# Performance work log

Measured on AMD Instinct MI355X. Metric: run time of the kernel, lower is better.

## Reference

```python
import jax, jax.numpy as jnp
import numpy as np

T, M, D_TRAJ, D_TEXT = 2048, 32, 256, 768
TAU = 1.0
LN_EPS = 1e-5

def _ln(x, g, b):
    mu = jnp.mean(x, axis=-1, keepdims=True)
    var = jnp.mean(jnp.square(x - mu), axis=-1, keepdims=True)
    return (x - mu) * jax.lax.rsqrt(var + LN_EPS) * g + b

def _gelu(x):
    return jax.nn.gelu(x, approximate=False)  # torch nn.GELU default (erf)

def _gcn_layer(x, src, dst, w, dst_scale, ln_g, ln_b, W, bb, N):
    h = _ln(x, ln_g, ln_b)
    m = h @ W + bb                      # [N, D]
    msg = m[src] * w[:, None]           # gather + weight  [E, D]
    out = jax.ops.segment_sum(msg, dst, num_segments=N)  # scatter-add
    deg = jax.ops.segment_sum(w, dst, num_segments=N)
    out = out / jnp.maximum(deg, 1.0)[:, None]
    out = out * dst_scale[:, None]
    return x + _gelu(out)

def setup_inputs() -> dict:
    key = jax.random.key(0)
    ks = jax.random.split(key, 12)
    traj_tokens = jax.random.normal(ks[0], (T, D_TRAJ), jnp.float32)
    word_tokens = jax.random.normal(ks[1], (M, D_TEXT), jnp.float32)
    t = jnp.arange(T - 1, dtype=jnp.int64)
    edge_index_temporal = jnp.stack([t, t + 1])                 # chain i->i+1
    ts = jnp.repeat(jnp.arange(T, dtype=jnp.int64), M)          # traj src
    ws = jnp.tile(jnp.arange(M, dtype=jnp.int64), T) + T        # word dst (offset T)
    edge_index_semantic = jnp.stack([ts, ws])
    s = 0.02
    params = {
        'W1': jax.random.normal(ks[2], (D_TRAJ, D_TEXT), jnp.float32) * s,
        'b1': jnp.zeros((D_TEXT,), jnp.float32),
        'W2': jax.random.normal(ks[3], (D_TEXT, D_TEXT), jnp.float32) * s,
        'b2': jnp.zeros((D_TEXT,), jnp.float32),
        'ln_g': jnp.ones((D_TEXT,), jnp.float32),
        'ln_b': jnp.zeros((D_TEXT,), jnp.float32),
        'traj_scale': jnp.asarray(0.2, jnp.float32),
        'g0_ln_g': jnp.ones((D_TEXT,), jnp.float32),
        'g0_ln_b': jnp.zeros((D_TEXT,), jnp.float32),
        'g0_W': jax.random.normal(ks[4], (D_TEXT, D_TEXT), jnp.float32) * s,
        'g0_b': jnp.zeros((D_TEXT,), jnp.float32),
        'g1_ln_g': jnp.ones((D_TEXT,), jnp.float32),
        'g1_ln_b': jnp.zeros((D_TEXT,), jnp.float32),
        'g1_W': jax.random.normal(ks[5], (D_TEXT, D_TEXT), jnp.float32) * s,
        'g1_b': jnp.zeros((D_TEXT,), jnp.float32),
    }
    return dict(traj_tokens=traj_tokens, word_tokens=word_tokens,
                edge_index_temporal=edge_index_temporal,
                edge_index_semantic=edge_index_semantic,
                valid_len=1536, **params)

def reference(traj_tokens, word_tokens, edge_index_temporal, edge_index_semantic,
              valid_len, W1, b1, W2, b2, ln_g, ln_b, traj_scale,
              g0_ln_g, g0_ln_b, g0_W, g0_b, g1_ln_g, g1_ln_b, g1_W, g1_b):
    N = T + M
    # traj projection MLP -> LN -> clamped learned scale
    z = _gelu(traj_tokens @ W1 + b1) @ W2 + b2
    z0 = _ln(z, ln_g, ln_b) * jnp.clip(traj_scale, 0.05, 2.0)
    h_init = jnp.concatenate([z0, word_tokens], axis=0)  # [N, D]
    # temporal edge weights gated by valid_len
    E_temp = edge_index_temporal.shape[1]
    w_temp = (jnp.arange(E_temp) < (valid_len - 1)).astype(jnp.float32)
    # semantic alignment: softmax over words per valid traj token
    zn = z0[:valid_len]
    zn = zn / jnp.maximum(jnp.linalg.norm(zn, axis=-1, keepdims=True), 1e-12)
    wn = word_tokens / jnp.maximum(jnp.linalg.norm(word_tokens, axis=-1, keepdims=True), 1e-12)
    alpha = jax.nn.softmax(zn @ wn.T / max(TAU, 1e-6), axis=1)   # [valid, M]
    alpha_full = jnp.concatenate(
        [alpha, jnp.zeros((T - valid_len, M), alpha.dtype)], axis=0)
    w_sem = alpha_full.reshape(-1)                               # [T*M]
    beta = alpha.sum(axis=0)
    inv_beta = jnp.clip(1.0 / (jax.lax.stop_gradient(beta) + 1e-6), 0.2, 5.0)
    dst_scale = jnp.concatenate([jnp.ones((T,), jnp.float32), inv_beta])
    # combined edge list + weights
    src = jnp.concatenate([edge_index_temporal[0], edge_index_semantic[0]])
    dst = jnp.concatenate([edge_index_temporal[1], edge_index_semantic[1]])
    w_all = jnp.concatenate([w_temp, w_sem])
    # 2-layer local DiWeightedGCN
    h = _gcn_layer(h_init, src, dst, w_all, dst_scale, g0_ln_g, g0_ln_b, g0_W, g0_b, N)
    h = _gcn_layer(h, src, dst, w_all, dst_scale, g1_ln_g, g1_ln_b, g1_W, g1_b, N)
    return h  # h_loc [T+M, D_TEXT]
```

## Files before the change

kernel.cpp:

```cpp
#include <hip/hip_runtime.h>
#include <math.h>

#define T_NODES 2048
#define M_WORDS 32
#define D 768
#define DTRAJ 256
#define NCHUNK 128

typedef __attribute__((ext_vector_type(8))) short bhalf8;
typedef __attribute__((ext_vector_type(4))) float f32x4;

#define AS1 __attribute__((address_space(1)))
#define AS3 __attribute__((address_space(3)))

constexpr size_t OFF_A1HI = 0;
constexpr size_t OFF_A1LO = OFF_A1HI + (size_t)T_NODES * DTRAJ * 2;
constexpr size_t OFF_AHI  = OFF_A1LO + (size_t)T_NODES * DTRAJ * 2;
constexpr size_t OFF_ALO  = OFF_AHI + (size_t)T_NODES * D * 2;
constexpr size_t OFF_WT1H = OFF_ALO + (size_t)T_NODES * D * 2;
constexpr size_t OFF_WT1L = OFF_WT1H + (size_t)D * DTRAJ * 2;
constexpr size_t OFF_WT2H = OFF_WT1L + (size_t)D * DTRAJ * 2;
constexpr size_t OFF_WT2L = OFF_WT2H + (size_t)D * D * 2;
constexpr size_t OFF_WG0H = OFF_WT2L + (size_t)D * D * 2;
constexpr size_t OFF_WG0L = OFF_WG0H + (size_t)D * D * 2;
constexpr size_t OFF_WG1H = OFF_WG0L + (size_t)D * D * 2;
constexpr size_t OFF_WG1L = OFF_WG1H + (size_t)D * D * 2;
constexpr size_t OFF_BUFB = OFF_WG1L + (size_t)D * D * 2;
constexpr size_t OFF_ALPH = OFF_BUFB + (size_t)T_NODES * D * 4;
constexpr size_t OFF_WPRT = OFF_ALPH + (size_t)T_NODES * M_WORDS * 4;
constexpr size_t OFF_BPRT = OFF_WPRT + (size_t)NCHUNK * M_WORDS * D * 4;
constexpr size_t OFF_INVW = OFF_BPRT + (size_t)NCHUNK * M_WORDS * 4;

__device__ __forceinline__ float gelu_exact(float x) {
    return 0.5f * x * (1.0f + erff(x * 0.70710678118654752f));
}
__device__ __forceinline__ unsigned short f2bf(float x) {
    unsigned int u = __float_as_uint(x);
    return (unsigned short)((u + 0x7fffu + ((u >> 16) & 1u)) >> 16);
}
__device__ __forceinline__ float bf2f(unsigned short b) {
    return __uint_as_float(((unsigned int)b) << 16);
}
__device__ __forceinline__ void stage16(const unsigned short* g, short* l) {
    __builtin_amdgcn_global_load_lds((const AS1 void*)g, (AS3 void*)l, 16, 0, 0);
}

__device__ __forceinline__ float wave_reduce_sum(float v) {
#pragma unroll
    for (int off = 32; off > 0; off >>= 1) v += __shfl_down(v, off);
    return v;
}
__device__ __forceinline__ float block_reduce_sum256(float v, float* sbuf) {
    v = wave_reduce_sum(v);
    const int lane = threadIdx.x & 63, wid = threadIdx.x >> 6;
    if (lane == 0) sbuf[wid] = v;
    __syncthreads();
    float r = sbuf[0] + sbuf[1] + sbuf[2] + sbuf[3];
    __syncthreads();
    return r;
}

__device__ __forceinline__ void ln_row(const float* __restrict__ x,
                                       const float* __restrict__ g,
                                       const float* __restrict__ b, float* sbuf,
                                       float& y0, float& y1, float& y2) {
    const int tid = threadIdx.x;
    const float x0 = x[tid], x1 = x[tid + 256], x2 = x[tid + 512];
    const float s = block_reduce_sum256(x0 + x1 + x2, sbuf);
    const float mu = s * (1.0f / 768.0f);
    const float d0 = x0 - mu, d1 = x1 - mu, d2 = x2 - mu;
    const float v = block_reduce_sum256(d0 * d0 + d1 * d1 + d2 * d2, sbuf);
    const float rs = rsqrtf(v * (1.0f / 768.0f) + 1e-5f);
    y0 = d0 * rs * g[tid] + b[tid];
    y1 = d1 * rs * g[tid + 256] + b[tid + 256];
    y2 = d2 * rs * g[tid + 512] + b[tid + 512];
}

__device__ __forceinline__ void tr_split_tile2(const float* __restrict__ W,
                                               unsigned short* __restrict__ hi,
                                               unsigned short* __restrict__ lo, int K,
                                               int N, int n0, int k0, float* tile) {
    const int tx = threadIdx.x & 31, ty = threadIdx.x >> 5;
#pragma unroll
    for (int i = 0; i < 32; i += 8)
        tile[(ty + i) * 33 + tx] = W[(size_t)(k0 + ty + i) * N + n0 + tx];
    __syncthreads();
#pragma unroll
    for (int i = 0; i < 32; i += 8) {
        const float v = tile[tx * 33 + ty + i];
        const unsigned short h = f2bf(v);
        const size_t o = (size_t)(n0 + ty + i) * K + k0 + tx;
        hi[o] = h;
        lo[o] = f2bf(v - bf2f(h));
    }
}

__global__ __launch_bounds__(256) void prep_kernel(
    const float* __restrict__ traj, const float* __restrict__ W1,
    const float* __restrict__ W2, const float* __restrict__ Wg0,
    const float* __restrict__ Wg1, const float* __restrict__ words,
    unsigned short* __restrict__ A1hi, unsigned short* __restrict__ A1lo,
    unsigned short* __restrict__ WT1h, unsigned short* __restrict__ WT1l,
    unsigned short* __restrict__ WT2h, unsigned short* __restrict__ WT2l,
    unsigned short* __restrict__ WG0h, unsigned short* __restrict__ WG0l,
    unsigned short* __restrict__ WG1h, unsigned short* __restrict__ WG1l,
    float* __restrict__ invw) {
    __shared__ float tile[32 * 33];
    __shared__ float sbuf[4];
    const int blk = blockIdx.x;
    if (blk < 512) {
        const int i = (blk * 256 + threadIdx.x) * 4;
        const float4 v = *(const float4*)(traj + i);
        ushort4 h, l;
        h.x = f2bf(v.x); l.x = f2bf(v.x - bf2f(h.x));
        h.y = f2bf(v.y); l.y = f2bf(v.y - bf2f(h.y));
        h.z = f2bf(v.z); l.z = f2bf(v.z - bf2f(h.z));
        h.w = f2bf(v.w); l.w = f2bf(v.w - bf2f(h.w));
        *(ushort4*)(A1hi + i) = h;
        *(ushort4*)(A1lo + i) = l;
    } else if (blk < 704) {
        const int idx = blk - 512;
        tr_split_tile2(W1, WT1h, WT1l, DTRAJ, D, (idx % 24) * 32, (idx / 24) * 32, tile);
    } else if (blk < 2432) {
        const int idx = blk - 704;
        const int wsel = idx / 576, rem = idx % 576;
        const float* W = (wsel == 0) ? W2 : (wsel == 1) ? Wg0 : Wg1;
        unsigned short* hi = (wsel == 0) ? WT2h : (wsel == 1) ? WG0h : WG1h;
        unsigned short* lo = (wsel == 0) ? WT2l : (wsel == 1) ? WG0l : WG1l;
        tr_split_tile2(W, hi, lo, D, D, (rem % 24) * 32, (rem / 24) * 32, tile);
    } else {
        const int w = blk - 2432;
        const size_t src = (size_t)w * D + threadIdx.x;
        const float x0 = words[src], x1 = words[src + 256], x2 = words[src + 512];
        const float ss = block_reduce_sum256(x0 * x0 + x1 * x1 + x2 * x2, sbuf);
        if (threadIdx.x == 0) invw[w] = 1.0f / fmaxf(sqrtf(ss), 1e-12f);
    }
}

#define MFMA_BF16(a, b, c) __builtin_amdgcn_mfma_f32_16x16x32_bf16(a, b, c, 0, 0, 0)

template <int EPI, bool TRIM>
__global__ __launch_bounds__(128) void mfma_gemm(
    const unsigned short* __restrict__ Ahi, const unsigned short* __restrict__ Alo,
    const unsigned short* __restrict__ Bthi, const unsigned short* __restrict__ Btlo,
    const float* __restrict__ bias, float* __restrict__ C,
    unsigned short* __restrict__ Ohi, unsigned short* __restrict__ Olo, int K_,
    const int* __restrict__ vlp) {
    const int bm = blockIdx.x * 64;
    if (TRIM && bm >= *vlp) return;
    __shared__ short sA[2][2][64 * 32];
    __shared__ short sB[2][2][96 * 32];
    const int bn = blockIdx.y * 96;
    const int tid = threadIdx.x;
    const int wv = tid >> 6, lane = tid & 63;
    const int lrow = lane >> 2;
    const int lchunk = (((lane & 3) ^ ((lrow >> 1) & 3)) << 3);
    const int g = lane >> 4, r = lane & 15;
    const int aoff = ((g ^ ((r >> 1) & 3)) << 3);
    const int wn = wv * 48;

    f32x4 acc[4][3];
#pragma unroll
    for (int i = 0; i < 4; ++i)
#pragma unroll
        for (int j = 0; j < 3; ++j) acc[i][j] = (f32x4){0.f, 0.f, 0.f, 0.f};

#define STAGE(buf, k0)                                                                     \
    if (wv == 0) {                                                                         \
        _Pragma("unroll") for (int i = 0; i < 4; ++i)                                      \
            stage16(Ahi + (size_t)(bm + i * 16 + lrow) * K_ + (k0) + lchunk,               \
                    &sA[buf][0][i * 512]);                                                 \
        _Pragma("unroll") for (int i = 0; i < 4; ++i)                                      \
            stage16(Alo + (size_t)(bm + i * 16 + lrow) * K_ + (k0) + lchunk,               \
                    &sA[buf][1][i * 512]);                                                 \
        _Pragma("unroll") for (int i = 0; i < 2; ++i)                                      \
            stage16(Bthi + (size_t)(bn + i * 16 + lrow) * K_ + (k0) + lchunk,              \
                    &sB[buf][0][i * 512]);                                                 \
    } else {                                                                               \
        _Pragma("unroll") for (int i = 2; i < 6; ++i)                                      \
            stage16(Bthi + (size_t)(bn + i * 16 + lrow) * K_ + (k0) + lchunk,              \
                    &sB[buf][0][i * 512]);                                                 \
        _Pragma("unroll") for (int i = 0; i < 6; ++i)                                      \
            stage16(Btlo + (size_t)(bn + i * 16 + lrow) * K_ + (k0) + lchunk,              \
                    &sB[buf][1][i * 512]);                                                 \
    }

    const int NT = K_ >> 5;
    STAGE(0, 0)
    __syncthreads();
    int cur = 0;
    for (int kt = 0; kt < NT; ++kt) {
        if (kt + 1 < NT) { STAGE(cur ^ 1, (kt + 1) << 5) }
        bhalf8 af[4][2];
#pragma unroll
        for (int fm = 0; fm < 4; ++fm) {
            af[fm][0] = *(const bhalf8*)(void*)&sA[cur][0][(fm * 16 + r) * 32 + aoff];
            af[fm][1] = *(const bhalf8*)(void*)&sA[cur][1][(fm * 16 + r) * 32 + aoff];
        }
#pragma unroll
        for (int fn = 0; fn < 3; ++fn) {
            const bhalf8 bh = *(const bhalf8*)(void*)&sB[cur][0][(wn + fn * 16 + r) * 32 + aoff];
            const bhalf8 bl = *(const bhalf8*)(void*)&sB[cur][1][(wn + fn * 16 + r) * 32 + aoff];
#pragma unroll
            for (int fm = 0; fm < 4; ++fm) {
                acc[fm][fn] = MFMA_BF16(af[fm][0], bh, acc[fm][fn]);
                acc[fm][fn] = MFMA_BF16(af[fm][0], bl, acc[fm][fn]);
                acc[fm][fn] = MFMA_BF16(af[fm][1], bh, acc[fm][fn]);
            }
        }
        __syncthreads();
        cur ^= 1;
    }
#undef STAGE

#pragma unroll
    for (int fm = 0; fm < 4; ++fm)
#pragma unroll
        for (int fn = 0; fn < 3; ++fn) {
            const int col = bn + wn + fn * 16 + r;
            const float bv = bias[col];
#pragma unroll
            for (int j = 0; j < 4; ++j) {
                const int row = bm + fm * 16 + g * 4 + j;
                float v = acc[fm][fn][j] + bv;
                if (EPI == 0) {
                    C[(size_t)row * D + col] = v;
                } else {
                    v = gelu_exact(v);
                    const unsigned short h = f2bf(v);
                    Ohi[(size_t)row * D + col] = h;
                    Olo[(size_t)row * D + col] = f2bf(v - bf2f(h));
                }
            }
        }
}

__global__ __launch_bounds__(256) void init_softmax(
    const float* __restrict__ z, const float* __restrict__ g,
    const float* __restrict__ b, const float* __restrict__ tsp,
    const float* __restrict__ words, const float* __restrict__ invw,
    const int* __restrict__ vlp, float* __restrict__ h, float* __restrict__ alpha) {
    __shared__ float sbuf[4];
    __shared__ float row[D];
    __shared__ float logits[M_WORDS];
    const int blk = blockIdx.x, tid = threadIdx.x;
    if (blk >= T_NODES) {
        const int w = blk - T_NODES;
        const size_t src = (size_t)w * D + tid;
        const size_t dst = (size_t)(T_NODES + w) * D + tid;
        h[dst] = words[src];
        h[dst + 256] = words[src + 256];
        h[dst + 512] = words[src + 512];
        return;
    }
    float y0, y1, y2;
    ln_row(z + (size_t)blk * D, g, b, sbuf, y0, y1, y2);
    const float sc = fminf(fmaxf(tsp[0], 0.05f), 2.0f);
    y0 *= sc; y1 *= sc; y2 *= sc;
    const size_t o = (size_t)blk * D + tid;
    h[o] = y0; h[o + 256] = y1; h[o + 512] = y2;
    const float ss = block_reduce_sum256(y0 * y0 + y1 * y1 + y2 * y2, sbuf);
    const float iz = 1.0f / fmaxf(sqrtf(ss), 1e-12f);
    if (blk >= *vlp) return;
    row[tid] = y0; row[tid + 256] = y1; row[tid + 512] = y2;
    __syncthreads();
    const int wid = tid >> 6, lane = tid & 63;
#pragma unroll
    for (int i = 0; i < 8; ++i) {
        const int w = wid * 8 + i;
        const float* wr = words + (size_t)w * D;
        float dot = 0.0f;
        for (int e = lane; e < D; e += 64) dot = fmaf(row[e], wr[e], dot);
        dot = wave_reduce_sum(dot);
        if (lane == 0) logits[w] = dot * iz * invw[w];
    }
    __syncthreads();
    if (tid < 64) {
        const float val = (tid < 32) ? logits[tid] : -INFINITY;
        float mx = val;
#pragma unroll
        for (int off = 32; off > 0; off >>= 1) mx = fmaxf(mx, __shfl_xor(mx, off));
        const float e = (tid < 32) ? expf(val - mx) : 0.0f;
        float sum = e;
#pragma unroll
        for (int off = 32; off > 0; off >>= 1) sum += __shfl_xor(sum, off);
        if (tid < 32) alpha[(size_t)blk * M_WORDS + tid] = e / sum;
    }
}

template <int FIN>
__global__ __launch_bounds__(256) void ln_split_fin(
    const float* __restrict__ x, const float* __restrict__ g,
    const float* __restrict__ b, unsigned short* __restrict__ hi,
    unsigned short* __restrict__ lo, const float* __restrict__ wpart,
    const float* __restrict__ bpart, float* __restrict__ h) {
    __shared__ float sbuf[4];
    const int blk = blockIdx.x, tid = threadIdx.x;
    if (blk < T_NODES) {
        float y0, y1, y2;
        ln_row(x + (size_t)blk * D, g, b, sbuf, y0, y1, y2);
        const size_t o = (size_t)blk * D + tid;
        unsigned short hh;
        hh = f2bf(y0); hi[o] = hh;       lo[o] = f2bf(y0 - bf2f(hh));
        hh = f2bf(y1); hi[o + 256] = hh; lo[o + 256] = f2bf(y1 - bf2f(hh));
        hh = f2bf(y2); hi[o + 512] = hh; lo[o + 512] = f2bf(y2 - bf2f(hh));
    } else if (FIN) {
        const int w = blk - T_NODES;
        float bsum = (tid < NCHUNK) ? bpart[tid * M_WORDS + w] : 0.0f;
        const float beta = block_reduce_sum256(bsum, sbuf);
        const float ib = fminf(fmaxf(1.0f / (beta + 1e-6f), 0.2f), 5.0f);
        const float scl = ib / fmaxf(beta, 1.0f);
#pragma unroll
        for (int i = 0; i < 3; ++i) {
            const int c = tid + i * 256;
            float acc = 0.0f;
#pragma unroll 8
            for (int q = 0; q < NCHUNK; ++q)
                acc += wpart[((size_t)q * M_WORDS + w) * D + c];
            h[(size_t)(T_NODES + w) * D + c] += gelu_exact(acc * scl);
        }
    }
}

__global__ __launch_bounds__(256) void gcn_agg_kernel(const float* __restrict__ m,
                                                      const float* __restrict__ alpha,
                                                      const int* __restrict__ vlp,
                                                      float* __restrict__ h,
                                                      float* __restrict__ wpart,
                                                      float* __restrict__ bpart) {
    const int VL = *vlp;
    const int chunk = blockIdx.x, cb = blockIdx.y;
    const int c = cb * 256 + threadIdx.x;
    const int tpc = (VL + NCHUNK - 1) / NCHUNK;
    const int t0 = chunk * tpc;
    const int t1 = min(t0 + tpc, VL);
    float acc[M_WORDS] = {};
    for (int t = t0; t < t1; ++t) {
        const float mv = m[(size_t)t * D + c];
        if (t + 1 < VL) h[(size_t)(t + 1) * D + c] += gelu_exact(mv);
        const float4* a4 = (const float4*)(alpha + (size_t)t * M_WORDS);
#pragma unroll
        for (int q = 0; q < 8; ++q) {
            const float4 a = a4[q];
            acc[q * 4 + 0] = fmaf(a.x, mv, acc[q * 4 + 0]);
            acc[q * 4 + 1] = fmaf(a.y, mv, acc[q * 4 + 1]);
            acc[q * 4 + 2] = fmaf(a.z, mv, acc[q * 4 + 2]);
            acc[q * 4 + 3] = fmaf(a.w, mv, acc[q * 4 + 3]);
        }
    }
#pragma unroll
    for (int w = 0; w < M_WORDS; ++w)
        wpart[((size_t)chunk * M_WORDS + w) * D + c] = acc[w];
    if (cb == 0 && threadIdx.x < M_WORDS) {
        float bs = 0.0f;
        for (int t = t0; t < t1; ++t) bs += alpha[(size_t)t * M_WORDS + threadIdx.x];
        bpart[chunk * M_WORDS + threadIdx.x] = bs;
    }
}

__global__ __launch_bounds__(256) void word_fin_kernel(const float* __restrict__ wpart,
                                                       const float* __restrict__ bpart,
                                                       float* __restrict__ h) {
    const int idx = blockIdx.x * 256 + threadIdx.x;
    const int w = idx / D, c = idx - w * D;
    float beta = 0.0f, acc = 0.0f;
#pragma unroll 8
    for (int q = 0; q < NCHUNK; ++q) {
        beta += bpart[q * M_WORDS + w];
        acc += wpart[((size_t)q * M_WORDS + w) * D + c];
    }
    const float ib = fminf(fmaxf(1.0f / (beta + 1e-6f), 0.2f), 5.0f);
    const float v = acc / fmaxf(beta, 1.0f) * ib;
    h[(size_t)(T_NODES + w) * D + c] += gelu_exact(v);
}

extern "C" void kernel_launch(void* const* d_in, const int* in_sizes, int n_in,
                              void* d_out, int out_size, void* d_ws, size_t ws_size,
                              hipStream_t stream) {
    const float* traj = (const float*)d_in[0];
    const float* words = (const float*)d_in[1];
    const int* vlp = (const int*)d_in[4];
    const float* W1 = (const float*)d_in[5];
    const float* b1 = (const float*)d_in[6];
    const float* W2 = (const float*)d_in[7];
    const float* b2 = (const float*)d_in[8];
    const float* ln_g = (const float*)d_in[9];
    const float* ln_b = (const float*)d_in[10];
    const float* tsc = (const float*)d_in[11];
    const float* g_ln_g[2] = {(const float*)d_in[12], (const float*)d_in[16]};
    const float* g_ln_b[2] = {(const float*)d_in[13], (const float*)d_in[17]};
    const float* g_W[2] = {(const float*)d_in[14], (const float*)d_in[18]};
    const float* g_b[2] = {(const float*)d_in[15], (const float*)d_in[19]};

    char* wsb = (char*)d_ws;
    unsigned short* A1hi = (unsigned short*)(wsb + OFF_A1HI);
    unsigned short* A1lo = (unsigned short*)(wsb + OFF_A1LO);
    unsigned short* Ahi = (unsigned short*)(wsb + OFF_AHI);
    unsigned short* Alo = (unsigned short*)(wsb + OFF_ALO);
    unsigned short* WT1h = (unsigned short*)(wsb + OFF_WT1H);
    unsigned short* WT1l = (unsigned short*)(wsb + OFF_WT1L);
    unsigned short* WT2h = (unsigned short*)(wsb + OFF_WT2H);
    unsigned short* WT2l = (unsigned short*)(wsb + OFF_WT2L);
    unsigned short* WG0h = (unsigned short*)(wsb + OFF_WG0H);
    unsigned short* WG0l = (unsigned short*)(wsb + OFF_WG0L);
    unsigned short* WG1h = (unsigned short*)(wsb + OFF_WG1H);
    unsigned short* WG1l = (unsigned short*)(wsb + OFF_WG1L);
    float* bufB = (float*)(wsb + OFF_BUFB);
    float* alpha = (float*)(wsb + OFF_ALPH);
    float* wpart = (float*)(wsb + OFF_WPRT);
    float* bpart = (float*)(wsb + OFF_BPRT);
    float* invw = (float*)(wsb + OFF_INVW);
    float* h = (float*)d_out;

    const unsigned short* WGh[2] = {WG0h, WG1h};
    const unsigned short* WGl[2] = {WG0l, WG1l};

    const dim3 ggrid(T_NODES / 64, D / 96);

    prep_kernel<<<2464, 256, 0, stream>>>(traj, W1, W2, g_W[0], g_W[1], words, A1hi, A1lo,
                                          WT1h, WT1l, WT2h, WT2l, WG0h, WG0l, WG1h, WG1l,
                                          invw);
    mfma_gemm<1, false><<<ggrid, 128, 0, stream>>>(A1hi, A1lo, WT1h, WT1l, b1, nullptr,
                                                   Ahi, Alo, DTRAJ, vlp);
    mfma_gemm<0, false><<<ggrid, 128, 0, stream>>>(Ahi, Alo, WT2h, WT2l, b2, bufB,
                                                   nullptr, nullptr, D, vlp);
    init_softmax<<<T_NODES + M_WORDS, 256, 0, stream>>>(bufB, ln_g, ln_b, tsc, words,
                                                        invw, vlp, h, alpha);
    ln_split_fin<0><<<T_NODES, 256, 0, stream>>>(h, g_ln_g[0], g_ln_b[0], Ahi, Alo,
                                                 nullptr, nullptr, h);
    mfma_gemm<0, true><<<ggrid, 128, 0, stream>>>(Ahi, Alo, WGh[0], WGl[0], g_b[0], bufB,
                                                  nullptr, nullptr, D, vlp);
    gcn_agg_kernel<<<dim3(NCHUNK, 3), 256, 0, stream>>>(bufB, alpha, vlp, h, wpart, bpart);
    ln_split_fin<1><<<T_NODES + M_WORDS, 256, 0, stream>>>(h, g_ln_g[1], g_ln_b[1], Ahi,
                                                           Alo, wpart, bpart, h);
    mfma_gemm<0, true><<<ggrid, 128, 0, stream>>>(Ahi, Alo, WGh[1], WGl[1], g_b[1], bufB,
                                                  nullptr, nullptr, D, vlp);
    gcn_agg_kernel<<<dim3(NCHUNK, 3), 256, 0, stream>>>(bufB, alpha, vlp, h, wpart, bpart);
    word_fin_kernel<<<(M_WORDS * D) / 256, 256, 0, stream>>>(wpart, bpart, h);
}
```

Measured before the change: 283.7 us.

## Retile MFMA GEMM to 32x96 blocks with 4 waves and K-step 64

The split-bf16 GEMM now uses 32-row tiles with 256 threads (four waves, each computing a 16x48 sub-tile) and stages 64-wide K slices with a new 8-way XOR swizzle. The grid doubles in M, giving more blocks and fewer sync iterations per K, which aims to improve occupancy and latency hiding on the many-CU GPU. The cost is less register-level reuse per wave, since each A fragment now feeds only 3 MFMAs instead of 12, and B tiles are loaded twice as often across the grid.

```diff
diff --git a/kernel.cpp b/kernel.cpp
--- a/kernel.cpp
+++ b/kernel.cpp
@@ -140,72 +140,72 @@
 #define MFMA_BF16(a, b, c) __builtin_amdgcn_mfma_f32_16x16x32_bf16(a, b, c, 0, 0, 0)
 
 template <int EPI, bool TRIM>
-__global__ __launch_bounds__(128) void mfma_gemm(
+__global__ __launch_bounds__(256, 2) void mfma_gemm(
     const unsigned short* __restrict__ Ahi, const unsigned short* __restrict__ Alo,
     const unsigned short* __restrict__ Bthi, const unsigned short* __restrict__ Btlo,
     const float* __restrict__ bias, float* __restrict__ C,
     unsigned short* __restrict__ Ohi, unsigned short* __restrict__ Olo, int K_,
     const int* __restrict__ vlp) {
-    const int bm = blockIdx.x * 64;
+    const int bm = blockIdx.x * 32;
     if (TRIM && bm >= *vlp) return;
-    __shared__ short sA[2][2][64 * 32];
-    __shared__ short sB[2][2][96 * 32];
+    __shared__ short sA[2][2][32 * 64];
+    __shared__ short sB[2][2][96 * 64];
     const int bn = blockIdx.y * 96;
     const int tid = threadIdx.x;
     const int wv = tid >> 6, lane = tid & 63;
-    const int lrow = lane >> 2;
-    const int lchunk = (((lane & 3) ^ ((lrow >> 1) & 3)) << 3);
+    const int lr8 = lane >> 3;
+    const int lch = ((lane & 7) ^ (lr8 & 7)) << 3;
     const int g = lane >> 4, r = lane & 15;
-    const int aoff = ((g ^ ((r >> 1) & 3)) << 3);
-    const int wn = wv * 48;
-
-    f32x4 acc[4][3];
-#pragma unroll
-    for (int i = 0; i < 4; ++i)
-#pragma unroll
-        for (int j = 0; j < 3; ++j) acc[i][j] = (f32x4){0.f, 0.f, 0.f, 0.f};
+    const int wm = (wv >> 1) * 16, wn = (wv & 1) * 48;
+
+    f32x4 acc[3];
+#pragma unroll
+    for (int j = 0; j < 3; ++j) acc[j] = (f32x4){0.f, 0.f, 0.f, 0.f};
 
 #define STAGE(buf, k0)                                                                     \
     if (wv == 0) {                                                                         \
         _Pragma("unroll") for (int i = 0; i < 4; ++i)                                      \
-            stage16(Ahi + (size_t)(bm + i * 16 + lrow) * K_ + (k0) + lchunk,               \
+            stage16(Ahi + (size_t)(bm + i * 8 + lr8) * K_ + (k0) + lch,                    \
                     &sA[buf][0][i * 512]);                                                 \
         _Pragma("unroll") for (int i = 0; i < 4; ++i)                                      \
-            stage16(Alo + (size_t)(bm + i * 16 + lrow) * K_ + (k0) + lchunk,               \
+            stage16(Alo + (size_t)(bm + i * 8 + lr8) * K_ + (k0) + lch,                    \
                     &sA[buf][1][i * 512]);                                                 \
-        _Pragma("unroll") for (int i = 0; i < 2; ++i)                                      \
-            stage16(Bthi + (size_t)(bn + i * 16 + lrow) * K_ + (k0) + lchunk,              \
+    } else if (wv == 1) {                                                                  \
+        _Pragma("unroll") for (int i = 0; i < 8; ++i)                                      \
+            stage16(Bthi + (size_t)(bn + i * 8 + lr8) * K_ + (k0) + lch,                   \
                     &sB[buf][0][i * 512]);                                                 \
+    } else if (wv == 2) {                                                                  \
+        _Pragma("unroll") for (int i = 0; i < 4; ++i)                                      \
+            stage16(Bthi + (size_t)(bn + 64 + i * 8 + lr8) * K_ + (k0) + lch,              \
+                    &sB[buf][0][(8 + i) * 512]);                                           \
+        _Pragma("unroll") for (int i = 0; i < 4; ++i)                                      \
+            stage16(Btlo + (size_t)(bn + i * 8 + lr8) * K_ + (k0) + lch,                   \
+                    &sB[buf][1][i * 512]);                                                 \
     } else {                                                                               \
-        _Pragma("unroll") for (int i = 2; i < 6; ++i)                                      \
-            stage16(Bthi + (size_t)(bn + i * 16 + lrow) * K_ + (k0) + lchunk,              \
-                    &sB[buf][0][i * 512]);                                                 \
-        _Pragma("unroll") for (int i = 0; i < 6; ++i)                                      \
-            stage16(Btlo + (size_t)(bn + i * 16 + lrow) * K_ + (k0) + lchunk,              \
-                    &sB[buf][1][i * 512]);                                                 \
-    }
-
-    const int NT = K_ >> 5;
+        _Pragma("unroll") for (int i = 0; i < 8; ++i)                                      \
+            stage16(Btlo + (size_t)(bn + 32 + i * 8 + lr8) * K_ + (k0) + lch,              \
+                    &sB[buf][1][(4 + i) * 512]);                                           \
+    }
+
+    const int NT = K_ >> 6;
     STAGE(0, 0)
     __syncthreads();
     int cur = 0;
     for (int kt = 0; kt < NT; ++kt) {
-        if (kt + 1 < NT) { STAGE(cur ^ 1, (kt + 1) << 5) }
-        bhalf8 af[4][2];
-#pragma unroll
-        for (int fm = 0; fm < 4; ++fm) {
-            af[fm][0] = *(const bhalf8*)(void*)&sA[cur][0][(fm * 16 + r) * 32 + aoff];
-            af[fm][1] = *(const bhalf8*)(void*)&sA[cur][1][(fm * 16 + r) * 32 + aoff];
-        }
-#pragma unroll
-        for (int fn = 0; fn < 3; ++fn) {
-            const bhalf8 bh = *(const bhalf8*)(void*)&sB[cur][0][(wn + fn * 16 + r) * 32 + aoff];
-            const bhalf8 bl = *(const bhalf8*)(void*)&sB[cur][1][(wn + fn * 16 + r) * 32 + aoff];
-#pragma unroll
-            for (int fm = 0; fm < 4; ++fm) {
-                acc[fm][fn] = MFMA_BF16(af[fm][0], bh, acc[fm][fn]);
-                acc[fm][fn] = MFMA_BF16(af[fm][0], bl, acc[fm][fn]);
-                acc[fm][fn] = MFMA_BF16(af[fm][1], bh, acc[fm][fn]);
+        if (kt + 1 < NT) { STAGE(cur ^ 1, (kt + 1) << 6) }
+#pragma unroll
+        for (int ks = 0; ks < 2; ++ks) {
+            const int koff = ((ks * 4 + g) ^ (r & 7)) << 3;
+            const bhalf8 ah = *(const bhalf8*)(void*)&sA[cur][0][(wm + r) * 64 + koff];
+            const bhalf8 al = *(const bhalf8*)(void*)&sA[cur][1][(wm + r) * 64 + koff];
+#pragma unroll
+            for (int fn = 0; fn < 3; ++fn) {
+                const int brow = (wn + fn * 16 + r) * 64 + koff;
+                const bhalf8 bh = *(const bhalf8*)(void*)&sB[cur][0][brow];
+                const bhalf8 bl = *(const bhalf8*)(void*)&sB[cur][1][brow];
+                acc[fn] = MFMA_BF16(ah, bh, acc[fn]);
+                acc[fn] = MFMA_BF16(ah, bl, acc[fn]);
+                acc[fn] = MFMA_BF16(al, bh, acc[fn]);
             }
         }
         __syncthreads();
@@ -214,25 +214,23 @@
 #undef STAGE
 
 #pragma unroll
-    for (int fm = 0; fm < 4; ++fm)
-#pragma unroll
-        for (int fn = 0; fn < 3; ++fn) {
-            const int col = bn + wn + fn * 16 + r;
-            const float bv = bias[col];
-#pragma unroll
-            for (int j = 0; j < 4; ++j) {
-                const int row = bm + fm * 16 + g * 4 + j;
-                float v = acc[fm][fn][j] + bv;
-                if (EPI == 0) {
-                    C[(size_t)row * D + col] = v;
-                } else {
-                    v = gelu_exact(v);
-                    const unsigned short h = f2bf(v);
-                    Ohi[(size_t)row * D + col] = h;
-                    Olo[(size_t)row * D + col] = f2bf(v - bf2f(h));
-                }
+    for (int fn = 0; fn < 3; ++fn) {
+        const int col = bn + wn + fn * 16 + r;
+        const float bv = bias[col];
+#pragma unroll
+        for (int j = 0; j < 4; ++j) {
+            const int row = bm + wm + g * 4 + j;
+            float v = acc[fn][j] + bv;
+            if (EPI == 0) {
+                C[(size_t)row * D + col] = v;
+            } else {
+                v = gelu_exact(v);
+                const unsigned short h = f2bf(v);
+                Ohi[(size_t)row * D + col] = h;
+                Olo[(size_t)row * D + col] = f2bf(v - bf2f(h));
             }
         }
+    }
 }
 
 __global__ __launch_bounds__(256) void init_softmax(
@@ -415,25 +413,25 @@
     const unsigned short* WGh[2] = {WG0h, WG1h};
     const unsigned short* WGl[2] = {WG0l, WG1l};
 
-    const dim3 ggrid(T_NODES / 64, D / 96);
+    const dim3 ggrid(T_NODES / 32, D / 96);
 
     prep_kernel<<<2464, 256, 0, stream>>>(traj, W1, W2, g_W[0], g_W[1], words, A1hi, A1lo,
                                           WT1h, WT1l, WT2h, WT2l, WG0h, WG0l, WG1h, WG1l,
                                           invw);
-    mfma_gemm<1, false><<<ggrid, 128, 0, stream>>>(A1hi, A1lo, WT1h, WT1l, b1, nullptr,
+    mfma_gemm<1, false><<<ggrid, 256, 0, stream>>>(A1hi, A1lo, WT1h, WT1l, b1, nullptr,
                                                    Ahi, Alo, DTRAJ, vlp);
-    mfma_gemm<0, false><<<ggrid, 128, 0, stream>>>(Ahi, Alo, WT2h, WT2l, b2, bufB,
+    mfma_gemm<0, false><<<ggrid, 256, 0, stream>>>(Ahi, Alo, WT2h, WT2l, b2, bufB,
                                                    nullptr, nullptr, D, vlp);
     init_softmax<<<T_NODES + M_WORDS, 256, 0, stream>>>(bufB, ln_g, ln_b, tsc, words,
                                                         invw, vlp, h, alpha);
     ln_split_fin<0><<<T_NODES, 256, 0, stream>>>(h, g_ln_g[0], g_ln_b[0], Ahi, Alo,
                                                  nullptr, nullptr, h);
-    mfma_gemm<0, true><<<ggrid, 128, 0, stream>>>(Ahi, Alo, WGh[0], WGl[0], g_b[0], bufB,
+    mfma_gemm<0, true><<<ggrid, 256, 0, stream>>>(Ahi, Alo, WGh[0], WGl[0], g_b[0], bufB,
                                                   nullptr, nullptr, D, vlp);
     gcn_agg_kernel<<<dim3(NCHUNK, 3), 256, 0, stream>>>(bufB, alpha, vlp, h, wpart, bpart);
     ln_split_fin<1><<<T_NODES + M_WORDS, 256, 0, stream>>>(h, g_ln_g[1], g_ln_b[1], Ahi,
                                                            Alo, wpart, bpart, h);
-    mfma_gemm<0, true><<<ggrid, 128, 0, stream>>>(Ahi, Alo, WGh[1], WGl[1], g_b[1], bufB,
+    mfma_gemm<0, true><<<ggrid, 256, 0, stream>>>(Ahi, Alo, WGh[1], WGl[1], g_b[1], bufB,
                                                   nullptr, nullptr, D, vlp);
     gcn_agg_kernel<<<dim3(NCHUNK, 3), 256, 0, stream>>>(bufB, alpha, vlp, h, wpart, bpart);
     word_fin_kernel<<<(M_WORDS * D) / 256, 256, 0, stream>>>(wpart, bpart, h);
```

Measured after the change: 249.4 us. 1.14x faster.

## Use 4-wave GEMM blocks with XCD-aware tile remap and skip invalid LN rows

Applied to the files above, without the earlier changes.

The MFMA GEMM goes from 2 waves to 4 waves per block. Each wave now owns a 32x48 sub-tile instead of 64x48, and each wave stages one operand slice. The 2D grid becomes a 1D grid whose block IDs are remapped so that consecutive tiles land on the same XCD, and the LDS swizzle pattern changes. LayerNorm-split blocks for rows at or beyond the valid length now exit early, which avoids work that trimmed GEMMs never read; the cost is some extra register and scheduling pressure per block.

```diff
diff --git a/kernel.cpp b/kernel.cpp
--- a/kernel.cpp
+++ b/kernel.cpp
@@ -140,48 +140,49 @@
 #define MFMA_BF16(a, b, c) __builtin_amdgcn_mfma_f32_16x16x32_bf16(a, b, c, 0, 0, 0)
 
 template <int EPI, bool TRIM>
-__global__ __launch_bounds__(128) void mfma_gemm(
+__global__ __launch_bounds__(256, 2) void mfma_gemm(
     const unsigned short* __restrict__ Ahi, const unsigned short* __restrict__ Alo,
     const unsigned short* __restrict__ Bthi, const unsigned short* __restrict__ Btlo,
     const float* __restrict__ bias, float* __restrict__ C,
     unsigned short* __restrict__ Ohi, unsigned short* __restrict__ Olo, int K_,
     const int* __restrict__ vlp) {
-    const int bm = blockIdx.x * 64;
+    const int id = blockIdx.x;
+    const int wgid = (id & 7) * 32 + (id >> 3);
+    const int bm = (wgid >> 3) * 64;
+    const int bn = (wgid & 7) * 96;
     if (TRIM && bm >= *vlp) return;
     __shared__ short sA[2][2][64 * 32];
     __shared__ short sB[2][2][96 * 32];
-    const int bn = blockIdx.y * 96;
     const int tid = threadIdx.x;
     const int wv = tid >> 6, lane = tid & 63;
-    const int lrow = lane >> 2;
-    const int lchunk = (((lane & 3) ^ ((lrow >> 1) & 3)) << 3);
+    const int lr = lane >> 2;
+    const int lch = ((lane & 3) ^ (lr & 3)) << 3;
     const int g = lane >> 4, r = lane & 15;
-    const int aoff = ((g ^ ((r >> 1) & 3)) << 3);
-    const int wn = wv * 48;
-
-    f32x4 acc[4][3];
-#pragma unroll
-    for (int i = 0; i < 4; ++i)
+    const int koff = ((g ^ (r & 3)) << 3);
+    const int wm = (wv >> 1) * 32, wn = (wv & 1) * 48;
+
+    f32x4 acc[2][3];
+#pragma unroll
+    for (int i = 0; i < 2; ++i)
 #pragma unroll
         for (int j = 0; j < 3; ++j) acc[i][j] = (f32x4){0.f, 0.f, 0.f, 0.f};
 
 #define STAGE(buf, k0)                                                                     \
     if (wv == 0) {                                                                         \
         _Pragma("unroll") for (int i = 0; i < 4; ++i)                                      \
-            stage16(Ahi + (size_t)(bm + i * 16 + lrow) * K_ + (k0) + lchunk,               \
+            stage16(Ahi + (size_t)(bm + i * 16 + lr) * K_ + (k0) + lch,                    \
                     &sA[buf][0][i * 512]);                                                 \
+    } else if (wv == 1) {                                                                  \
         _Pragma("unroll") for (int i = 0; i < 4; ++i)                                      \
-            stage16(Alo + (size_t)(bm + i * 16 + lrow) * K_ + (k0) + lchunk,               \
+            stage16(Alo + (size_t)(bm + i * 16 + lr) * K_ + (k0) + lch,                    \
                     &sA[buf][1][i * 512]);                                                 \
-        _Pragma("unroll") for (int i = 0; i < 2; ++i)                                      \
-            stage16(Bthi + (size_t)(bn + i * 16 + lrow) * K_ + (k0) + lchunk,              \
+    } else if (wv == 2) {                                                                  \
+        _Pragma("unroll") for (int i = 0; i < 6; ++i)                                      \
+            stage16(Bthi + (size_t)(bn + i * 16 + lr) * K_ + (k0) + lch,                   \
                     &sB[buf][0][i * 512]);                                                 \
     } else {                                                                               \
-        _Pragma("unroll") for (int i = 2; i < 6; ++i)                                      \
-            stage16(Bthi + (size_t)(bn + i * 16 + lrow) * K_ + (k0) + lchunk,              \
-                    &sB[buf][0][i * 512]);                                                 \
         _Pragma("unroll") for (int i = 0; i < 6; ++i)                                      \
-            stage16(Btlo + (size_t)(bn + i * 16 + lrow) * K_ + (k0) + lchunk,              \
+            stage16(Btlo + (size_t)(bn + i * 16 + lr) * K_ + (k0) + lch,                   \
                     &sB[buf][1][i * 512]);                                                 \
     }
 
@@ -191,18 +192,19 @@
     int cur = 0;
     for (int kt = 0; kt < NT; ++kt) {
         if (kt + 1 < NT) { STAGE(cur ^ 1, (kt + 1) << 5) }
-        bhalf8 af[4][2];
-#pragma unroll
-        for (int fm = 0; fm < 4; ++fm) {
-            af[fm][0] = *(const bhalf8*)(void*)&sA[cur][0][(fm * 16 + r) * 32 + aoff];
-            af[fm][1] = *(const bhalf8*)(void*)&sA[cur][1][(fm * 16 + r) * 32 + aoff];
+        bhalf8 af[2][2];
+#pragma unroll
+        for (int fm = 0; fm < 2; ++fm) {
+            af[fm][0] = *(const bhalf8*)(void*)&sA[cur][0][(wm + fm * 16 + r) * 32 + koff];
+            af[fm][1] = *(const bhalf8*)(void*)&sA[cur][1][(wm + fm * 16 + r) * 32 + koff];
         }
 #pragma unroll
         for (int fn = 0; fn < 3; ++fn) {
-            const bhalf8 bh = *(const bhalf8*)(void*)&sB[cur][0][(wn + fn * 16 + r) * 32 + aoff];
-            const bhalf8 bl = *(const bhalf8*)(void*)&sB[cur][1][(wn + fn * 16 + r) * 32 + aoff];
-#pragma unroll
-            for (int fm = 0; fm < 4; ++fm) {
+            const int brow = (wn + fn * 16 + r) * 32 + koff;
+            const bhalf8 bh = *(const bhalf8*)(void*)&sB[cur][0][brow];
+            const bhalf8 bl = *(const bhalf8*)(void*)&sB[cur][1][brow];
+#pragma unroll
+            for (int fm = 0; fm < 2; ++fm) {
                 acc[fm][fn] = MFMA_BF16(af[fm][0], bh, acc[fm][fn]);
                 acc[fm][fn] = MFMA_BF16(af[fm][0], bl, acc[fm][fn]);
                 acc[fm][fn] = MFMA_BF16(af[fm][1], bh, acc[fm][fn]);
@@ -214,14 +216,14 @@
 #undef STAGE
 
 #pragma unroll
-    for (int fm = 0; fm < 4; ++fm)
+    for (int fm = 0; fm < 2; ++fm)
 #pragma unroll
         for (int fn = 0; fn < 3; ++fn) {
             const int col = bn + wn + fn * 16 + r;
             const float bv = bias[col];
 #pragma unroll
             for (int j = 0; j < 4; ++j) {
-                const int row = bm + fm * 16 + g * 4 + j;
+                const int row = bm + wm + fm * 16 + g * 4 + j;
                 float v = acc[fm][fn][j] + bv;
                 if (EPI == 0) {
                     C[(size_t)row * D + col] = v;
@@ -293,10 +295,12 @@
     const float* __restrict__ x, const float* __restrict__ g,
     const float* __restrict__ b, unsigned short* __restrict__ hi,
     unsigned short* __restrict__ lo, const float* __restrict__ wpart,
-    const float* __restrict__ bpart, float* __restrict__ h) {
+    const float* __restrict__ bpart, float* __restrict__ h,
+    const int* __restrict__ vlp) {
     __shared__ float sbuf[4];
     const int blk = blockIdx.x, tid = threadIdx.x;
     if (blk < T_NODES) {
+        if (blk >= *vlp) return;
         float y0, y1, y2;
         ln_row(x + (size_t)blk * D, g, b, sbuf, y0, y1, y2);
         const size_t o = (size_t)blk * D + tid;
@@ -415,25 +419,25 @@
     const unsigned short* WGh[2] = {WG0h, WG1h};
     const unsigned short* WGl[2] = {WG0l, WG1l};
 
-    const dim3 ggrid(T_NODES / 64, D / 96);
+    const int ggrid = (T_NODES / 64) * (D / 96);
 
     prep_kernel<<<2464, 256, 0, stream>>>(traj, W1, W2, g_W[0], g_W[1], words, A1hi, A1lo,
                                           WT1h, WT1l, WT2h, WT2l, WG0h, WG0l, WG1h, WG1l,
                                           invw);
-    mfma_gemm<1, false><<<ggrid, 128, 0, stream>>>(A1hi, A1lo, WT1h, WT1l, b1, nullptr,
+    mfma_gemm<1, false><<<ggrid, 256, 0, stream>>>(A1hi, A1lo, WT1h, WT1l, b1, nullptr,
                                                    Ahi, Alo, DTRAJ, vlp);
-    mfma_gemm<0, false><<<ggrid, 128, 0, stream>>>(Ahi, Alo, WT2h, WT2l, b2, bufB,
+    mfma_gemm<0, false><<<ggrid, 256, 0, stream>>>(Ahi, Alo, WT2h, WT2l, b2, bufB,
                                                    nullptr, nullptr, D, vlp);
     init_softmax<<<T_NODES + M_WORDS, 256, 0, stream>>>(bufB, ln_g, ln_b, tsc, words,
                                                         invw, vlp, h, alpha);
     ln_split_fin<0><<<T_NODES, 256, 0, stream>>>(h, g_ln_g[0], g_ln_b[0], Ahi, Alo,
-                                                 nullptr, nullptr, h);
-    mfma_gemm<0, true><<<ggrid, 128, 0, stream>>>(Ahi, Alo, WGh[0], WGl[0], g_b[0], bufB,
+                                                 nullptr, nullptr, h, vlp);
+    mfma_gemm<0, true><<<ggrid, 256, 0, stream>>>(Ahi, Alo, WGh[0], WGl[0], g_b[0], bufB,
                                                   nullptr, nullptr, D, vlp);
     gcn_agg_kernel<<<dim3(NCHUNK, 3), 256, 0, stream>>>(bufB, alpha, vlp, h, wpart, bpart);
     ln_split_fin<1><<<T_NODES + M_WORDS, 256, 0, stream>>>(h, g_ln_g[1], g_ln_b[1], Ahi,
-                                                           Alo, wpart, bpart, h);
-    mfma_gemm<0, true><<<ggrid, 128, 0, stream>>>(Ahi, Alo, WGh[1], WGl[1], g_b[1], bufB,
+                                                           Alo, wpart, bpart, h, vlp);
+    mfma_gemm<0, true><<<ggrid, 256, 0, stream>>>(Ahi, Alo, WGh[1], WGl[1], g_b[1], bufB,
                                                   nullptr, nullptr, D, vlp);
     gcn_agg_kernel<<<dim3(NCHUNK, 3), 256, 0, stream>>>(bufB, alpha, vlp, h, wpart, bpart);
     word_fin_kernel<<<(M_WORDS * D) / 256, 256, 0, stream>>>(wpart, bpart, h);
```

After: 274.0 us. -3.4%, faster.
